# Kernel optimization log

Hardware: AMD Instinct MI355X
Metric: run time of the kernel (lower is better)

The kernel has to match this reference:

```python
import jax, jax.numpy as jnp
import numpy as np

D, H, DK, DF = 512, 8, 64, 2048  # dim, heads, head_dim, forward_dim
EPS = 1e-5


def _layernorm(x, g, b):
    mu = jnp.mean(x, axis=-1, keepdims=True)
    var = jnp.mean(jnp.square(x - mu), axis=-1, keepdims=True)
    return (x - mu) * jax.lax.rsqrt(var + EPS) * g + b


def setup_inputs() -> dict:
    key = jax.random.key(0)
    ks = jax.random.split(key, 16)
    B, S = 2, 2048
    s_in = 1.0 / np.sqrt(D)
    s_ff = 1.0 / np.sqrt(DF)
    s_cat = 1.0 / np.sqrt(H * DK)
    return {
        "x": jax.random.normal(ks[0], (B, S, D), jnp.float32),
        # per-head Q/K/V projections stacked over heads: [H, D, DK]
        "Wq": jax.random.uniform(ks[1], (H, D, DK), jnp.float32, -s_in, s_in),
        "bq": jax.random.uniform(ks[2], (H, DK), jnp.float32, -s_in, s_in),
        "Wk": jax.random.uniform(ks[3], (H, D, DK), jnp.float32, -s_in, s_in),
        "bk": jax.random.uniform(ks[4], (H, DK), jnp.float32, -s_in, s_in),
        "Wv": jax.random.uniform(ks[5], (H, D, DK), jnp.float32, -s_in, s_in),
        "bv": jax.random.uniform(ks[6], (H, DK), jnp.float32, -s_in, s_in),
        "Wo": jax.random.uniform(ks[7], (H * DK, D), jnp.float32, -s_cat, s_cat),
        "bo": jax.random.uniform(ks[8], (D,), jnp.float32, -s_cat, s_cat),
        "ln1_g": jnp.ones((D,), jnp.float32),
        "ln1_b": jnp.zeros((D,), jnp.float32),
        "W1": jax.random.uniform(ks[9], (D, DF), jnp.float32, -s_in, s_in),
        "b1": jax.random.uniform(ks[10], (DF,), jnp.float32, -s_in, s_in),
        "W2": jax.random.uniform(ks[11], (DF, D), jnp.float32, -s_ff, s_ff),
        "b2": jax.random.uniform(ks[12], (D,), jnp.float32, -s_ff, s_ff),
        "ln2_g": jnp.ones((D,), jnp.float32),
        "ln2_b": jnp.zeros((D,), jnp.float32),
    }


def reference(x, Wq, bq, Wk, bk, Wv, bv, Wo, bo, ln1_g, ln1_b, W1, b1, W2, b2, ln2_g, ln2_b):
    # Per-head projections, batched over heads: [B,H,S,DK]
    q = jnp.einsum('bsd,hdk->bhsk', x, Wq) + bq[None, :, None, :]
    k = jnp.einsum('bsd,hdk->bhsk', x, Wk) + bk[None, :, None, :]
    v = jnp.einsum('bsd,hdk->bhsk', x, Wv) + bv[None, :, None, :]
    scale = 1.0 / np.sqrt(DK)
    scores = jnp.einsum('bhsk,bhtk->bhst', q, k) * scale  # [B,H,S,S]
    attn = jax.nn.softmax(scores, axis=-1)
    o = jnp.einsum('bhst,bhtk->bhsk', attn, v)  # [B,H,S,DK]
    # concat heads (head order matches torch cat over ModuleList)
    B, _, S, _ = o.shape
    o = o.transpose(0, 2, 1, 3).reshape(B, S, H * DK)
    attn_out = o @ Wo + bo
    # Residual 1 (dropout = identity in eval): LN(x + sublayer(x))
    h = _layernorm(x + attn_out, ln1_g, ln1_b)
    # FeedForward + Residual 2
    ff = jax.nn.relu(h @ W1 + b1) @ W2 + b2
    return _layernorm(h + ff, ln2_g, ln2_b)
```

## Files before the change

kernel.cpp:

```cpp
#include <hip/hip_runtime.h>


#define Dm   512
#define Hh   8
#define DKk  64
#define DFf  2048
#define Bb   2
#define Ss   2048
#define Nn   4096

typedef __attribute__((ext_vector_type(8))) short short8;
typedef __attribute__((ext_vector_type(4))) float f32x4;
typedef __attribute__((ext_vector_type(2))) float f32x2;
typedef __attribute__((ext_vector_type(4))) short short4v;
typedef __attribute__((ext_vector_type(2))) int   int2v;

__device__ inline float bf2f(short s) {
    unsigned u = ((unsigned)(unsigned short)s) << 16;
    float f; __builtin_memcpy(&f, &u, 4); return f;
}
__device__ inline void bf2x2(unsigned v, float& a, float& b) {
    unsigned ua = v << 16, ub = v & 0xffff0000u;
    __builtin_memcpy(&a, &ua, 4); __builtin_memcpy(&b, &ub, 4);
}
__device__ inline short f2bf(float f) {
    unsigned u; __builtin_memcpy(&u, &f, 4);
    u = (u + 0x7fff + ((u >> 16) & 1)) >> 16;
    return (short)u;
}
__device__ inline short cvt_elem(const void* p, long i, int f32flag) {
    if (f32flag) return f2bf(((const float*)p)[i]);
    return ((const short*)p)[i];
}
__device__ inline int detect_f32(const void* x) {
    const float* xf = (const float*)x;
    int ok = 0;
#pragma unroll
    for (int i = 0; i < 16; ++i) {
        float a = fabsf(xf[i]);
        ok += (a > 1e-8f && a < 1e4f) ? 1 : 0;
    }
    return ok >= 8;
}
__device__ inline void gload_lds16(const short* g, short* l) {
    __builtin_amdgcn_global_load_lds(
        (const __attribute__((address_space(1))) unsigned int*)g,
        (__attribute__((address_space(3))) unsigned int*)l, 16, 0, 0);
}

__global__ __launch_bounds__(256) void prep_kernel(
    const void* __restrict__ x, short* __restrict__ xb,
    const void* bq, const void* bk, const void* bv, const void* bo,
    const void* b1, const void* b2, const void* g1, const void* be1,
    const void* g2, const void* be2, short* __restrict__ smalls,
    const void* Wq, const void* Wk, const void* Wv,
    const void* Wo, const void* W1, const void* W2,
    short* __restrict__ WqkvT,
    short* __restrict__ WoT, short* __restrict__ W1T, short* __restrict__ W2T)
{
    const int f = detect_f32(x);
    int blk = blockIdx.x;
    if (blk < 512) {
        long base = (long)blk * 4096;
        if (f) {
            const float* xf = (const float*)x;
#pragma unroll
            for (int j = 0; j < 4; ++j) {
                int off = threadIdx.x * 4 + j * 1024;
                f32x4 v = *(const f32x4*)(xf + base + off);
                short4v s4;
#pragma unroll
                for (int i2 = 0; i2 < 4; ++i2) s4[i2] = f2bf(v[i2]);
                *(short4v*)(xb + base + off) = s4;
            }
        } else {
            const short* xs = (const short*)x;
#pragma unroll
            for (int j = 0; j < 2; ++j) {
                int off = threadIdx.x * 8 + j * 2048;
                *(short8*)(xb + base + off) = *(const short8*)(xs + base + off);
            }
        }
        return;
    }
    if (blk == 512) {
        const void* srcs[10] = {bq, bk, bv, bo, b1, b2, g1, be1, g2, be2};
        const int   sz[10]   = {512, 512, 512, 512, 2048, 512, 512, 512, 512, 512};
        int off = 0;
        for (int j = 0; j < 10; ++j) {
            for (int i = threadIdx.x; i < sz[j]; i += 256)
                smalls[off + i] = cvt_elem(srcs[j], i, f);
            off += sz[j];
        }
        return;
    }
    __shared__ short tile[64][65];
    blk -= 513;
    const void* src; short* dst; long srcoff = 0; long dstoff = 0; int R, C, tr, tc;
    if (blk < 192) {
        int m = blk >> 6; int r = blk & 63; int h = r >> 3; int t = r & 7;
        src = (m == 0) ? Wq : (m == 1) ? Wk : Wv;
        dst = WqkvT + (long)m * 512 * 512;
        srcoff = (long)h * 512 * 64; dstoff = (long)h * 64 * 512;
        R = 512; C = 64; tr = t; tc = 0;
    } else if (blk < 256) {
        int r = blk - 192; src = Wo; dst = WoT; R = 512; C = 512; tr = r >> 3; tc = r & 7;
    } else if (blk < 512) {
        int r = blk - 256; src = W1; dst = W1T; R = 512; C = 2048; tr = r >> 5; tc = r & 31;
    } else {
        int r = blk - 512; src = W2; dst = W2T; R = 2048; C = 512; tr = r >> 3; tc = r & 7;
    }
    int r0 = tr * 64, c0 = tc * 64;
    for (int i = threadIdx.x; i < 4096; i += 256) {
        int rr = i >> 6, cc = i & 63;
        tile[rr][cc] = cvt_elem(src, srcoff + (long)(r0 + rr) * C + c0 + cc, f);
    }
    __syncthreads();
    for (int i = threadIdx.x; i < 4096; i += 256) {
        int cc = i >> 6, rr = i & 63;
        dst[dstoff + (long)(c0 + cc) * R + r0 + rr] = tile[rr][cc];
    }
}

#define MODE_PART_BF16 1
#define MODE_RELU_BF16 2
#define MODE_QKV       4

#define QSCALE 0.18033688011112042f

__global__ __launch_bounds__(256) void gemm_kernel(
    const short* __restrict__ A, const short* __restrict__ Bt,
    const short* __restrict__ bias, void* __restrict__ outp,
    void* __restrict__ out2, void* __restrict__ out3,
    int K, int Ncols, int mode, int Ktile)
{
    __shared__ short As[2][128 * 64];
    __shared__ short Bs[2][128 * 64];
    const int t    = threadIdx.x;
    const int lane = t & 63;
    const int wave = t >> 6;
    const int quad = lane >> 4;
    const int l15  = lane & 15;
    const int wm = wave >> 1, wn = wave & 1;
    const int row0 = blockIdx.x * 128;
    const int col0 = blockIdx.y * 128;
    const int kbase = blockIdx.z * Ktile;

    const int ri = lane >> 3;
    const int ct = (lane & 7) ^ ri;

    f32x4 acc[4][4];
#pragma unroll
    for (int i = 0; i < 4; ++i)
#pragma unroll
        for (int j = 0; j < 4; ++j) acc[i][j] = (f32x4){0.f, 0.f, 0.f, 0.f};

    auto stage = [&](int buf, int k0) {
#pragma unroll
        for (int p = 0; p < 4; ++p) {
            int r = wave * 32 + p * 8;
            gload_lds16(A + (long)(row0 + r + ri) * K + kbase + k0 + ct * 8,
                        &As[buf][r * 64 + lane * 8]);
        }
#pragma unroll
        for (int p = 0; p < 4; ++p) {
            int r = wave * 32 + p * 8;
            gload_lds16(Bt + (long)(col0 + r + ri) * K + kbase + k0 + ct * 8,
                        &Bs[buf][r * 64 + lane * 8]);
        }
    };

    stage(0, 0);
    int cur = 0;
    const int niter = Ktile >> 6;
    for (int it = 0; it < niter; ++it) {
        asm volatile("s_waitcnt vmcnt(0)" ::: "memory");
        __syncthreads();
        if (it + 1 < niter) stage(cur ^ 1, (it + 1) * 64);
#pragma unroll
        for (int kk = 0; kk < 2; ++kk) {
            short8 af[4], bfr[4];
#pragma unroll
            for (int mt = 0; mt < 4; ++mt) {
                int rowa = wm * 64 + mt * 16 + l15;
                af[mt] = *(const short8*)&As[cur][rowa * 64
                              + (((kk * 4 + quad) ^ (rowa & 7)) * 8)];
            }
#pragma unroll
            for (int nt = 0; nt < 4; ++nt) {
                int rowb = wn * 64 + nt * 16 + l15;
                bfr[nt] = *(const short8*)&Bs[cur][rowb * 64
                              + (((kk * 4 + quad) ^ (rowb & 7)) * 8)];
            }
#pragma unroll
            for (int mt = 0; mt < 4; ++mt)
#pragma unroll
                for (int nt = 0; nt < 4; ++nt)
                    acc[mt][nt] = __builtin_amdgcn_mfma_f32_16x16x32_bf16(
                        af[mt], bfr[nt], acc[mt][nt], 0, 0, 0);
        }
        cur ^= 1;
    }

    const int wrow0 = row0 + wm * 64;
    const int wcol0 = col0 + wn * 64;
    if (mode == MODE_QKV) {
        int m = wcol0 >> 9;
        if (m < 2) {
            short* out = (short*)(m == 0 ? outp : out2);
            float sc = (m == 0) ? QSCALE : 1.0f;
#pragma unroll
            for (int nt = 0; nt < 4; ++nt) {
                int col = wcol0 + nt * 16 + l15;
                float bb = bf2f(bias[col]);
                int cl = col & 511;
#pragma unroll
                for (int mt = 0; mt < 4; ++mt)
#pragma unroll
                    for (int r = 0; r < 4; ++r) {
                        int row = wrow0 + mt * 16 + quad * 4 + r;
                        out[(long)row * 512 + cl] = f2bf((acc[mt][nt][r] + bb) * sc);
                    }
            }
        } else {
            short* out = (short*)out3;
#pragma unroll
            for (int nt = 0; nt < 4; ++nt) {
                int col = wcol0 + nt * 16 + l15;
                float bb = bf2f(bias[col]);
                int cl = col - 1024;
                int h = cl >> 6, kk = cl & 63;
#pragma unroll
                for (int mt = 0; mt < 4; ++mt) {
                    int row = wrow0 + mt * 16 + quad * 4;
                    int b = row >> 11, s = row & 2047;
                    short4v v4;
#pragma unroll
                    for (int r = 0; r < 4; ++r) v4[r] = f2bf(acc[mt][nt][r] + bb);
                    *(short4v*)&out[((long)(b * Hh + h) * DKk + kk) * Ss + s] = v4;
                }
            }
        }
    } else if (mode == MODE_PART_BF16) {
        short* out = (short*)outp + (long)blockIdx.z * Nn * Ncols;
        int zb = (blockIdx.z == 0);
#pragma unroll
        for (int nt = 0; nt < 4; ++nt) {
            int col = wcol0 + nt * 16 + l15;
            float bb = zb ? bf2f(bias[col]) : 0.f;
#pragma unroll
            for (int mt = 0; mt < 4; ++mt)
#pragma unroll
                for (int r = 0; r < 4; ++r) {
                    int row = wrow0 + mt * 16 + quad * 4 + r;
                    out[(long)row * Ncols + col] = f2bf(acc[mt][nt][r] + bb);
                }
        }
    } else {
        short* out = (short*)outp;
#pragma unroll
        for (int nt = 0; nt < 4; ++nt) {
            int col = wcol0 + nt * 16 + l15;
            float bb = bf2f(bias[col]);
#pragma unroll
            for (int mt = 0; mt < 4; ++mt)
#pragma unroll
                for (int r = 0; r < 4; ++r) {
                    int row = wrow0 + mt * 16 + quad * 4 + r;
                    out[(long)row * Ncols + col] = f2bf(fmaxf(acc[mt][nt][r] + bb, 0.f));
                }
        }
    }
}

__global__ __launch_bounds__(256) void attn_kernel(
    const short* __restrict__ Q, const short* __restrict__ Kt,
    const short* __restrict__ Vt, short* __restrict__ po, float* __restrict__ ls)
{
    __shared__ __align__(16) short Ks[64 * 64];
    __shared__ __align__(16) short Vs[64 * 64];
    __shared__ __align__(16) short pbuf[4][32 * 72];
    const int lane = threadIdx.x & 63;
    const int wave = threadIdx.x >> 6;
    const int quad = lane >> 4;
    const int l15  = lane & 15;
    const int qt = blockIdx.x, bh = blockIdx.y, ks = blockIdx.z;
    const int b = bh >> 3, h = bh & 7;
    const int qrow = b * Ss + qt * 128 + wave * 32;

    short8 bq[2][2];
#pragma unroll
    for (int qh = 0; qh < 2; ++qh)
#pragma unroll
        for (int kk = 0; kk < 2; ++kk)
            bq[qh][kk] = *(const short8*)(Q + (long)(qrow + qh * 16 + l15) * Dm
                                          + h * DKk + kk * 32 + quad * 8);

    short8 ones;
#pragma unroll
    for (int i = 0; i < 8; ++i) ones[i] = (short)0x3F80;

    f32x4 o[2][4];
    f32x4 olsum[2];
#pragma unroll
    for (int qh = 0; qh < 2; ++qh) {
        olsum[qh] = (f32x4){0.f, 0.f, 0.f, 0.f};
#pragma unroll
        for (int nt = 0; nt < 4; ++nt) o[qh][nt] = (f32x4){0.f, 0.f, 0.f, 0.f};
    }

    const short* Kg = Kt + (long)b * Ss * Dm + h * DKk;
    const short* Vg = Vt + (long)bh * DKk * Ss;
    short* pbw = pbuf[wave];
    const int t00 = ks * 512;

    const int ri = lane >> 3;
    const int ct = (lane & 7) ^ ri;
    const int ldsrow0 = wave * 16;

    for (int it = 0; it < 8; ++it) {
        const int t0 = t00 + it * 64;
#pragma unroll
        for (int p = 0; p < 2; ++p) {
            int r = ldsrow0 + p * 8 + ri;
            gload_lds16(Kg + (long)(t0 + r) * Dm + ct * 8,
                        &Ks[(ldsrow0 + p * 8) * 64] + lane * 8);
        }
#pragma unroll
        for (int p = 0; p < 2; ++p) {
            int r = ldsrow0 + p * 8 + ri;
            gload_lds16(Vg + (long)r * Ss + t0 + ct * 8,
                        &Vs[(ldsrow0 + p * 8) * 64] + lane * 8);
        }
        asm volatile("s_waitcnt vmcnt(0)" ::: "memory");
        __syncthreads();

#pragma unroll
        for (int j = 0; j < 4; ++j) {
            short8 kf0 = *(const short8*)&Ks[(j * 16 + l15) * 64
                                             + ((quad ^ (l15 & 7)) * 8)];
            short8 kf1 = *(const short8*)&Ks[(j * 16 + l15) * 64
                                             + (((4 + quad) ^ (l15 & 7)) * 8)];
#pragma unroll
            for (int qh = 0; qh < 2; ++qh) {
                f32x4 sj = (f32x4){0.f, 0.f, 0.f, 0.f};
                sj = __builtin_amdgcn_mfma_f32_16x16x32_bf16(kf0, bq[qh][0], sj, 0, 0, 0);
                sj = __builtin_amdgcn_mfma_f32_16x16x32_bf16(kf1, bq[qh][1], sj, 0, 0, 0);
                int2v pk;
#pragma unroll
                for (int r2 = 0; r2 < 2; ++r2) {
                    float pa = __builtin_amdgcn_exp2f(sj[r2 * 2 + 0]);
                    float pc = __builtin_amdgcn_exp2f(sj[r2 * 2 + 1]);
                    unsigned ua, uc;
                    __builtin_memcpy(&ua, &pa, 4);
                    __builtin_memcpy(&uc, &pc, 4);
                    pk[r2] = __builtin_amdgcn_perm(uc, ua, 0x07060302);
                }
                *(int2v*)&pbw[(qh * 16 + l15) * 72 + j * 16 + quad * 4] = pk;
            }
        }
        asm volatile("s_waitcnt lgkmcnt(0)" ::: "memory");
#pragma unroll
        for (int c = 0; c < 2; ++c) {
            short8 ap[2];
#pragma unroll
            for (int qh = 0; qh < 2; ++qh) {
                ap[qh] = *(const short8*)&pbw[(qh * 16 + l15) * 72 + c * 32 + quad * 8];
                olsum[qh] = __builtin_amdgcn_mfma_f32_16x16x32_bf16(
                    ap[qh], ones, olsum[qh], 0, 0, 0);
            }
#pragma unroll
            for (int nt = 0; nt < 4; ++nt) {
                short8 vf = *(const short8*)&Vs[(nt * 16 + l15) * 64
                                                + (((c * 4 + quad) ^ (l15 & 7)) * 8)];
#pragma unroll
                for (int qh = 0; qh < 2; ++qh)
                    o[qh][nt] = __builtin_amdgcn_mfma_f32_16x16x32_bf16(
                        ap[qh], vf, o[qh][nt], 0, 0, 0);
            }
        }
        asm volatile("" ::: "memory");
        __syncthreads();
    }

    short* pob = po + ((((long)bh * 16 + qt) * 4 + ks) * 128) * 64;
#pragma unroll
    for (int qh = 0; qh < 2; ++qh)
#pragma unroll
        for (int nt = 0; nt < 4; ++nt)
#pragma unroll
            for (int r = 0; r < 4; ++r)
                pob[(wave * 32 + qh * 16 + quad * 4 + r) * 64 + nt * 16 + l15] =
                    f2bf(o[qh][nt][r]);
    if (l15 == 0) {
        long lbase = (((long)bh * 16 + qt) * 4 + ks) * 128 + wave * 32;
#pragma unroll
        for (int qh = 0; qh < 2; ++qh)
            *(f32x4*)&ls[lbase + qh * 16 + quad * 4] = olsum[qh];
    }
}

__global__ __launch_bounds__(256) void combine_kernel(
    const short* __restrict__ po, const float* __restrict__ ls,
    short* __restrict__ O)
{
    const int qt = blockIdx.x, bh = blockIdx.y;
    const int b = bh >> 3, h = bh & 7;
    const long base = ((long)bh * 16 + qt) * 4;
    const int tid = threadIdx.x;
    const int qloc = tid >> 4;
    const int dk0 = (tid & 15) * 4;
#pragma unroll
    for (int q0 = 0; q0 < 8; ++q0) {
        int q = q0 * 16 + qloc;
        f32x4 s = (f32x4){0.f, 0.f, 0.f, 0.f};
        float L = 0.f;
#pragma unroll
        for (int ksp = 0; ksp < 4; ++ksp) {
            short4v pv = *(const short4v*)(po + ((base + ksp) * 128 + q) * 64 + dk0);
#pragma unroll
            for (int i = 0; i < 4; ++i) s[i] += bf2f(pv[i]);
            L += ls[(base + ksp) * 128 + q];
        }
        float inv = 1.f / L;
        short4v ov;
#pragma unroll
        for (int i = 0; i < 4; ++i) ov[i] = f2bf(s[i] * inv);
        *(short4v*)(O + (long)(b * Ss + qt * 128 + q) * Dm + h * DKk + dk0) = ov;
    }
}

__global__ __launch_bounds__(256) void ln_kernel(
    const short* __restrict__ v0, const short* __restrict__ v1,
    const short* __restrict__ v2, const short* __restrict__ v3,
    const short* res,
    const short* __restrict__ g, const short* __restrict__ bt,
    void* out, const void* __restrict__ xdet)
{
    const int row = blockIdx.x, tid = threadIdx.x;
    const long base = (long)row * Dm;
    const int e0 = tid * 2;
    float x0, x1;
    { unsigned v = *(const unsigned*)(res + base + e0); bf2x2(v, x0, x1); }
    { unsigned v = *(const unsigned*)(v0 + base + e0);
      float a, c; bf2x2(v, a, c); x0 += a; x1 += c; }
    if (v1) { unsigned v = *(const unsigned*)(v1 + base + e0);
              float a, c; bf2x2(v, a, c); x0 += a; x1 += c; }
    if (v2) { unsigned v = *(const unsigned*)(v2 + base + e0);
              float a, c; bf2x2(v, a, c); x0 += a; x1 += c; }
    if (v3) { unsigned v = *(const unsigned*)(v3 + base + e0);
              float a, c; bf2x2(v, a, c); x0 += a; x1 += c; }

    __shared__ float red[8];
    const int wv = tid >> 6, ln = tid & 63;
    float s = x0 + x1;
#pragma unroll
    for (int mk = 1; mk < 64; mk <<= 1) s += __shfl_xor(s, mk);
    if (!ln) red[wv] = s;
    __syncthreads();
    float mean = (red[0] + red[1] + red[2] + red[3]) * (1.f / 512.f);
    float d0 = x0 - mean, d1 = x1 - mean;
    float q = d0 * d0 + d1 * d1;
#pragma unroll
    for (int mk = 1; mk < 64; mk <<= 1) q += __shfl_xor(q, mk);
    if (!ln) red[4 + wv] = q;
    __syncthreads();
    float rs = rsqrtf((red[4] + red[5] + red[6] + red[7]) * (1.f / 512.f) + 1e-5f);
    float ga, gb, ba, bb;
    { unsigned v = *(const unsigned*)(g + e0);  bf2x2(v, ga, gb); }
    { unsigned v = *(const unsigned*)(bt + e0); bf2x2(v, ba, bb); }
    float y0 = d0 * rs * ga + ba;
    float y1 = d1 * rs * gb + bb;
    int f32out = xdet ? detect_f32(xdet) : 0;
    if (f32out) {
        *(f32x2*)((float*)out + base + e0) = (f32x2){y0, y1};
    } else {
        short* o = (short*)out;
        unsigned pk = (unsigned)(unsigned short)f2bf(y0)
                    | ((unsigned)(unsigned short)f2bf(y1) << 16);
        *(unsigned*)(o + base + e0) = pk;
    }
}

extern "C" void kernel_launch(void* const* d_in, const int* in_sizes, int n_in,
                              void* d_out, int out_size, void* d_ws, size_t ws_size,
                              hipStream_t stream)
{
    (void)in_sizes; (void)n_in; (void)out_size; (void)ws_size;
    const void* x   = d_in[0];
    const void* Wq  = d_in[1];  const void* bq  = d_in[2];
    const void* Wk  = d_in[3];  const void* bk  = d_in[4];
    const void* Wv  = d_in[5];  const void* bv  = d_in[6];
    const void* Wo  = d_in[7];  const void* bo  = d_in[8];
    const void* g1  = d_in[9];  const void* be1 = d_in[10];
    const void* W1  = d_in[11]; const void* b1  = d_in[12];
    const void* W2  = d_in[13]; const void* b2  = d_in[14];
    const void* g2  = d_in[15]; const void* be2 = d_in[16];

    char* ws = (char*)d_ws;
    size_t off = 0;
    auto alloc = [&](size_t bytes) -> void* {
        void* p = ws + off; off += (bytes + 255) & ~(size_t)255; return p;
    };
    short* WqkvT = (short*)alloc((size_t)3 * Dm * Dm * 2);
    short* WoT   = (short*)alloc((size_t)Dm * Dm * 2);
    short* W1T   = (short*)alloc((size_t)DFf * Dm * 2);
    short* W2T   = (short*)alloc((size_t)Dm * DFf * 2);
    short* xb    = (short*)alloc((size_t)Nn * Dm * 2);
    short* sm    = (short*)alloc((size_t)6656 * 2);
    char*  regA  = (char*)alloc((size_t)Nn * DFf * 2);
    short* Qb    = (short*)(regA);
    short* Kb    = (short*)(regA + (size_t)Nn * Dm * 2);
    short* Vt    = (short*)(regA + (size_t)Nn * Dm * 4);
    short* Ob    = (short*)(regA + (size_t)Nn * Dm * 6);
    short* u     = (short*)(regA);
    char*  regC  = (char*)alloc((size_t)4 * Nn * Dm * 2 * 2);
    short* po    = (short*)regC;
    short* wo_p  = (short*)regC;
    short* f2p   = (short*)regC;
    float* lsb   = (float*)alloc((size_t)16 * 16 * 4 * 128 * 4);
    short* h_bf  = xb;

    prep_kernel<<<1281, 256, 0, stream>>>(x, xb, bq, bk, bv, bo, b1, b2,
                                          g1, be1, g2, be2, sm,
                                          Wq, Wk, Wv, Wo, W1, W2,
                                          WqkvT, WoT, W1T, W2T);
    gemm_kernel<<<dim3(Nn / 128, 1536 / 128, 1), 256, 0, stream>>>(
        xb, WqkvT, sm + 0, Qb, Kb, Vt, Dm, 1536, MODE_QKV, Dm);
    attn_kernel<<<dim3(Ss / 128, Bb * Hh, 4), 256, 0, stream>>>(Qb, Kb, Vt, po, lsb);
    combine_kernel<<<dim3(Ss / 128, Bb * Hh), 256, 0, stream>>>(po, lsb, Ob);
    gemm_kernel<<<dim3(Nn / 128, Dm / 128, 2), 256, 0, stream>>>(
        Ob, WoT, sm + 1536, wo_p, nullptr, nullptr, Dm, Dm, MODE_PART_BF16, Dm / 2);
    ln_kernel<<<Nn, 256, 0, stream>>>(wo_p, wo_p + (long)Nn * Dm, nullptr, nullptr,
                                      xb, sm + 4608, sm + 5120, h_bf, nullptr);
    gemm_kernel<<<dim3(Nn / 128, DFf / 128, 1), 256, 0, stream>>>(
        h_bf, W1T, sm + 2048, u, nullptr, nullptr, Dm, DFf, MODE_RELU_BF16, Dm);
    gemm_kernel<<<dim3(Nn / 128, Dm / 128, 4), 256, 0, stream>>>(
        u, W2T, sm + 4096, f2p, nullptr, nullptr, DFf, Dm, MODE_PART_BF16, DFf / 4);
    ln_kernel<<<Nn, 256, 0, stream>>>(f2p, f2p + (long)Nn * Dm, f2p + (long)2 * Nn * Dm,
                                      f2p + (long)3 * Nn * Dm,
                                      h_bf, sm + 5632, sm + 6144, d_out, x);
}
```

Before: 201.2 us.

## Fuse split-K attention combine into the output-projection GEMM A-tile load

Removes the separate combine kernel and instead has a dedicated Wo GEMM kernel read the four split-K partial attention outputs and their row sums, normalize them in registers, and write the combined bf16 A tile straight to LDS. This drops one kernel launch and the write/read round trip of the combined O buffer. In exchange, each Wo block redoes the combine for its row tile across the four column blocks, so partial data is re-read four times. wo_p moves to its own allocation because po now stays live while wo_p is being written.

```diff
diff --git a/kernel.cpp b/kernel.cpp
--- a/kernel.cpp
+++ b/kernel.cpp
@@ -273,6 +273,133 @@
     }
 }
 
+__global__ __launch_bounds__(256) void wo_gemm_kernel(
+    const short* __restrict__ po, const float* __restrict__ ls,
+    const short* __restrict__ Bt, const short* __restrict__ bias,
+    short* __restrict__ outp)
+{
+    __shared__ short As[2][128 * 64];
+    __shared__ short Bs[2][128 * 64];
+    const int t    = threadIdx.x;
+    const int lane = t & 63;
+    const int wave = t >> 6;
+    const int quad = lane >> 4;
+    const int l15  = lane & 15;
+    const int wm = wave >> 1, wn = wave & 1;
+    const int row0 = blockIdx.x * 128;
+    const int col0 = blockIdx.y * 128;
+    const int z    = blockIdx.z;
+    const int b    = row0 >> 11;
+    const int qtl  = (row0 >> 7) & 15;
+
+    const int ri = lane >> 3;
+    const int ct = (lane & 7) ^ ri;
+
+    f32x4 acc[4][4];
+#pragma unroll
+    for (int i = 0; i < 4; ++i)
+#pragma unroll
+        for (int j = 0; j < 4; ++j) acc[i][j] = (f32x4){0.f, 0.f, 0.f, 0.f};
+
+    auto stageB = [&](int buf, int k0) {
+#pragma unroll
+        for (int p = 0; p < 4; ++p) {
+            int r = wave * 32 + p * 8;
+            gload_lds16(Bt + (long)(col0 + r + ri) * Dm + z * 256 + k0 + ct * 8,
+                        &Bs[buf][r * 64 + lane * 8]);
+        }
+    };
+
+    short8 pv[4][4];
+    float  Lv[4];
+    auto loadA = [&](int it) {
+        int h = z * 4 + it;
+        long tb = ((long)((b * Hh + h) * 16 + qtl)) * 4;
+        const short* pob = po + tb * 128 * 64;
+        const float* lsb = ls + tb * 128;
+#pragma unroll
+        for (int p = 0; p < 4; ++p) {
+            int q = wave * 32 + p * 8 + ri;
+            float L = 0.f;
+#pragma unroll
+            for (int ks = 0; ks < 4; ++ks) {
+                pv[p][ks] = *(const short8*)(pob + ((long)ks * 128 + q) * 64 + ct * 8);
+                L += lsb[ks * 128 + q];
+            }
+            Lv[p] = L;
+        }
+    };
+    auto finishA = [&](int buf) {
+#pragma unroll
+        for (int p = 0; p < 4; ++p) {
+            int r = wave * 32 + p * 8;
+            float inv = 1.f / Lv[p];
+            short8 a8;
+#pragma unroll
+            for (int e = 0; e < 8; ++e) {
+                float s = bf2f(pv[p][0][e]) + bf2f(pv[p][1][e])
+                        + bf2f(pv[p][2][e]) + bf2f(pv[p][3][e]);
+                a8[e] = f2bf(s * inv);
+            }
+            *(short8*)&As[buf][r * 64 + lane * 8] = a8;
+        }
+    };
+
+    loadA(0);
+    stageB(0, 0);
+    finishA(0);
+    int cur = 0;
+    for (int it = 0; it < 4; ++it) {
+        asm volatile("s_waitcnt vmcnt(0)" ::: "memory");
+        __syncthreads();
+        if (it < 3) {
+            loadA(it + 1);
+            stageB(cur ^ 1, (it + 1) * 64);
+        }
+#pragma unroll
+        for (int kk = 0; kk < 2; ++kk) {
+            short8 af[4], bfr[4];
+#pragma unroll
+            for (int mt = 0; mt < 4; ++mt) {
+                int rowa = wm * 64 + mt * 16 + l15;
+                af[mt] = *(const short8*)&As[cur][rowa * 64
+                              + (((kk * 4 + quad) ^ (rowa & 7)) * 8)];
+            }
+#pragma unroll
+            for (int nt = 0; nt < 4; ++nt) {
+                int rowb = wn * 64 + nt * 16 + l15;
+                bfr[nt] = *(const short8*)&Bs[cur][rowb * 64
+                              + (((kk * 4 + quad) ^ (rowb & 7)) * 8)];
+            }
+#pragma unroll
+            for (int mt = 0; mt < 4; ++mt)
+#pragma unroll
+                for (int nt = 0; nt < 4; ++nt)
+                    acc[mt][nt] = __builtin_amdgcn_mfma_f32_16x16x32_bf16(
+                        af[mt], bfr[nt], acc[mt][nt], 0, 0, 0);
+        }
+        if (it < 3) finishA(cur ^ 1);
+        cur ^= 1;
+    }
+
+    const int wrow0 = row0 + wm * 64;
+    const int wcol0 = col0 + wn * 64;
+    short* out = outp + (long)z * Nn * Dm;
+    int zb = (z == 0);
+#pragma unroll
+    for (int nt = 0; nt < 4; ++nt) {
+        int col = wcol0 + nt * 16 + l15;
+        float bb = zb ? bf2f(bias[col]) : 0.f;
+#pragma unroll
+        for (int mt = 0; mt < 4; ++mt)
+#pragma unroll
+            for (int r = 0; r < 4; ++r) {
+                int row = wrow0 + mt * 16 + quad * 4 + r;
+                out[(long)row * Dm + col] = f2bf(acc[mt][nt][r] + bb);
+            }
+    }
+}
+
 __global__ __launch_bounds__(256) void attn_kernel(
     const short* __restrict__ Q, const short* __restrict__ Kt,
     const short* __restrict__ Vt, short* __restrict__ po, float* __restrict__ ls)
@@ -397,36 +524,6 @@
 #pragma unroll
         for (int qh = 0; qh < 2; ++qh)
             *(f32x4*)&ls[lbase + qh * 16 + quad * 4] = olsum[qh];
-    }
-}
-
-__global__ __launch_bounds__(256) void combine_kernel(
-    const short* __restrict__ po, const float* __restrict__ ls,
-    short* __restrict__ O)
-{
-    const int qt = blockIdx.x, bh = blockIdx.y;
-    const int b = bh >> 3, h = bh & 7;
-    const long base = ((long)bh * 16 + qt) * 4;
-    const int tid = threadIdx.x;
-    const int qloc = tid >> 4;
-    const int dk0 = (tid & 15) * 4;
-#pragma unroll
-    for (int q0 = 0; q0 < 8; ++q0) {
-        int q = q0 * 16 + qloc;
-        f32x4 s = (f32x4){0.f, 0.f, 0.f, 0.f};
-        float L = 0.f;
-#pragma unroll
-        for (int ksp = 0; ksp < 4; ++ksp) {
-            short4v pv = *(const short4v*)(po + ((base + ksp) * 128 + q) * 64 + dk0);
-#pragma unroll
-            for (int i = 0; i < 4; ++i) s[i] += bf2f(pv[i]);
-            L += ls[(base + ksp) * 128 + q];
-        }
-        float inv = 1.f / L;
-        short4v ov;
-#pragma unroll
-        for (int i = 0; i < 4; ++i) ov[i] = f2bf(s[i] * inv);
-        *(short4v*)(O + (long)(b * Ss + qt * 128 + q) * Dm + h * DKk + dk0) = ov;
     }
 }
 
@@ -512,12 +609,11 @@
     short* Qb    = (short*)(regA);
     short* Kb    = (short*)(regA + (size_t)Nn * Dm * 2);
     short* Vt    = (short*)(regA + (size_t)Nn * Dm * 4);
-    short* Ob    = (short*)(regA + (size_t)Nn * Dm * 6);
     short* u     = (short*)(regA);
     char*  regC  = (char*)alloc((size_t)4 * Nn * Dm * 2 * 2);
     short* po    = (short*)regC;
-    short* wo_p  = (short*)regC;
     short* f2p   = (short*)regC;
+    short* wo_p  = (short*)alloc((size_t)2 * Nn * Dm * 2);
     float* lsb   = (float*)alloc((size_t)16 * 16 * 4 * 128 * 4);
     short* h_bf  = xb;
 
@@ -528,9 +624,8 @@
     gemm_kernel<<<dim3(Nn / 128, 1536 / 128, 1), 256, 0, stream>>>(
         xb, WqkvT, sm + 0, Qb, Kb, Vt, Dm, 1536, MODE_QKV, Dm);
     attn_kernel<<<dim3(Ss / 128, Bb * Hh, 4), 256, 0, stream>>>(Qb, Kb, Vt, po, lsb);
-    combine_kernel<<<dim3(Ss / 128, Bb * Hh), 256, 0, stream>>>(po, lsb, Ob);
-    gemm_kernel<<<dim3(Nn / 128, Dm / 128, 2), 256, 0, stream>>>(
-        Ob, WoT, sm + 1536, wo_p, nullptr, nullptr, Dm, Dm, MODE_PART_BF16, Dm / 2);
+    wo_gemm_kernel<<<dim3(Nn / 128, Dm / 128, 2), 256, 0, stream>>>(
+        po, lsb, WoT, sm + 1536, wo_p);
     ln_kernel<<<Nn, 256, 0, stream>>>(wo_p, wo_p + (long)Nn * Dm, nullptr, nullptr,
                                       xb, sm + 4608, sm + 5120, h_bf, nullptr);
     gemm_kernel<<<dim3(Nn / 128, DFf / 128, 1), 256, 0, stream>>>(
```

Measured after the change: 199.4 us (median of 2 runs). About the same (-0.9%).
